# Performance work log

Measured on AMD Instinct MI355X. Metric: run time of the kernel, lower is better.

Reference implementation:

```python
import jax, jax.numpy as jnp
import numpy as np

DIM = 384
NUM_HEADS = 8
HEAD_DIM = DIM // NUM_HEADS
SCALE = HEAD_DIM ** -0.5
MLP_HIDDEN = int(DIM * 4.0)
EPS = 1e-6


def setup_inputs() -> dict:
    key = jax.random.key(0)
    ks = jax.random.split(key, 8)
    s = 0.02
    return {
        "x": jax.random.normal(ks[0], (2, DIM, 8, 16, 16), dtype=jnp.float32),
        "g1": jnp.ones((DIM,), jnp.float32),
        "b1": jnp.zeros((DIM,), jnp.float32),
        "Wqkv": jax.random.normal(ks[1], (DIM, 3 * DIM), jnp.float32) * s,  # no bias (qkv_bias=False)
        "Wo": jax.random.normal(ks[2], (DIM, DIM), jnp.float32) * s,
        "bo": jnp.zeros((DIM,), jnp.float32),
        "g2": jnp.ones((DIM,), jnp.float32),
        "b2": jnp.zeros((DIM,), jnp.float32),
        "W1": jax.random.normal(ks[3], (DIM, MLP_HIDDEN), jnp.float32) * s,
        "b1m": jnp.zeros((MLP_HIDDEN,), jnp.float32),
        "W2": jax.random.normal(ks[4], (MLP_HIDDEN, DIM), jnp.float32) * s,
        "b2m": jnp.zeros((DIM,), jnp.float32),
    }


def _layernorm(x, g, b):
    mu = jnp.mean(x, axis=-1, keepdims=True)
    var = jnp.mean(jnp.square(x - mu), axis=-1, keepdims=True)
    return (x - mu) * jax.lax.rsqrt(var + EPS) * g + b


def _attention(h, Wqkv, Wo, bo):
    B, N, C = h.shape
    qkv = h @ Wqkv  # [B, N, 3C]
    qkv = qkv.reshape(B, N, 3, NUM_HEADS, HEAD_DIM).transpose(2, 0, 3, 1, 4)
    q, k, v = qkv[0], qkv[1], qkv[2]  # each [B, H, N, d]
    att = jax.nn.softmax(jnp.einsum('bhxd,bhyd->bhxy', q, k) * SCALE, axis=-1)
    out = jnp.einsum('bhxy,bhyd->bhxd', att, v)  # [B, H, N, d]
    out = out.transpose(0, 2, 1, 3).reshape(B, N, C)
    return out @ Wo + bo


def reference(x, g1, b1, Wqkv, Wo, bo, g2, b2, W1, b1m, W2, b2m):
    B, C, D, H, W = x.shape
    h = x.transpose(0, 2, 3, 4, 1).reshape(B, D * H * W, C)  # b (d h w) c
    h = h + _attention(_layernorm(h, g1, b1), Wqkv, Wo, bo)
    m = _layernorm(h, g2, b2)
    m = jax.nn.gelu(m @ W1 + b1m, approximate=False) @ W2 + b2m
    h = h + m
    return h.reshape(B, D, H, W, C).transpose(0, 4, 1, 2, 3)
```

## Files before the change

### kernel.cpp

```cpp
#include <hip/hip_runtime.h>
#include <hip/hip_bf16.h>
#include <math.h>

#define DIM    384
#define NHEAD  8
#define HDIM   48
#define NTOK   2048
#define BATCH  2
#define TOKS   (BATCH * NTOK)
#define HIDDEN 1536

typedef __bf16 bf16x8 __attribute__((ext_vector_type(8)));
typedef float  f32x4  __attribute__((ext_vector_type(4)));
typedef unsigned short u16;

union bfu { __hip_bfloat16 h; u16 u; };

__device__ __forceinline__ void load_lds16(const void* g, void* l) {
    __builtin_amdgcn_global_load_lds(
        (const __attribute__((address_space(1))) void*)g,
        (__attribute__((address_space(3))) void*)l, 16, 0, 0);
}

__global__ __launch_bounds__(256) void wtrans_all(
    const float* __restrict__ Wqkv, const float* __restrict__ Wo,
    const float* __restrict__ W1,   const float* __restrict__ W2,
    __hip_bfloat16* __restrict__ WqkvT, __hip_bfloat16* __restrict__ WoT,
    __hip_bfloat16* __restrict__ W1T,   __hip_bfloat16* __restrict__ W2T) {
    __shared__ float t[32][33];
    int id = blockIdx.x;
    const float* src; __hip_bfloat16* dst; int R, C;
    if (id < 432)       { src = Wqkv; dst = WqkvT; R = 384;  C = 1152; }
    else if (id < 576)  { id -= 432;  src = Wo;    dst = WoT;  R = 384;  C = 384; }
    else if (id < 1152) { id -= 576;  src = W1;    dst = W1T;  R = 384;  C = 1536; }
    else                { id -= 1152; src = W2;    dst = W2T;  R = 1536; C = 384; }
    int tc = C / 32;
    int i0 = (id / tc) * 32, j0 = (id % tc) * 32;
    int tx = threadIdx.x & 31, ty = threadIdx.x >> 5;
#pragma unroll
    for (int k = 0; k < 32; k += 8)
        t[ty + k][tx] = src[(size_t)(i0 + ty + k) * C + j0 + tx];
    __syncthreads();
#pragma unroll
    for (int k = 0; k < 32; k += 8)
        dst[(size_t)(j0 + ty + k) * R + i0 + tx] = __float2bfloat16(t[tx][ty + k]);
}

__global__ __launch_bounds__(256) void tln(const float* __restrict__ x,
                                           const float* __restrict__ g,
                                           const float* __restrict__ bta,
                                           float* __restrict__ hOut,
                                           __hip_bfloat16* __restrict__ y) {
    __shared__ float t[384 * 33];
    int n0 = blockIdx.x * 32, b = blockIdx.y;
    const float* xb = x + (size_t)b * DIM * NTOK;
    int tid = threadIdx.x;
    for (int idx = tid; idx < 384 * 32; idx += 256) {
        int c = idx >> 5, n = idx & 31;
        t[c * 33 + n] = xb[(size_t)c * NTOK + n0 + n];
    }
    __syncthreads();
    int wid = tid >> 6, lane = tid & 63;
#pragma unroll
    for (int it = 0; it < 8; ++it) {
        int tl = it * 4 + wid;
        float v[6];
        float s = 0.f;
#pragma unroll
        for (int i = 0; i < 6; ++i) { v[i] = t[(lane + 64 * i) * 33 + tl]; s += v[i]; }
#pragma unroll
        for (int o = 32; o; o >>= 1) s += __shfl_xor(s, o, 64);
        float mu = s * (1.f / DIM);
        float s2 = 0.f;
#pragma unroll
        for (int i = 0; i < 6; ++i) { float d = v[i] - mu; s2 += d * d; }
#pragma unroll
        for (int o = 32; o; o >>= 1) s2 += __shfl_xor(s2, o, 64);
        float r = rsqrtf(s2 * (1.f / DIM) + 1e-6f);
        size_t tok = (size_t)b * NTOK + n0 + tl;
#pragma unroll
        for (int i = 0; i < 6; ++i) {
            int c = lane + 64 * i;
            hOut[tok * DIM + c] = v[i];
            y[tok * DIM + c] = __float2bfloat16((v[i] - mu) * r * g[c] + bta[c]);
        }
    }
}

__global__ __launch_bounds__(256) void vtile(const u16* __restrict__ qkv,
                                             unsigned int* __restrict__ vt32) {
    __shared__ u16 t[128 * 49];
    int k0 = blockIdx.x * 128;
    int bh = blockIdx.y;
    int b = bh >> 3, h = bh & 7;
    int tid = threadIdx.x;
    const u16* src = qkv + (size_t)(b * NTOK + k0) * 1152 + 768 + h * 48;
#pragma unroll
    for (int idx = tid; idx < 768; idx += 256) {
        int r = idx / 6, c = idx % 6;
        uint4 v = *(const uint4*)(src + (size_t)r * 1152 + c * 8);
        u16* dst = &t[r * 49 + c * 8];
        dst[0] = (u16)(v.x & 0xffff); dst[1] = (u16)(v.x >> 16);
        dst[2] = (u16)(v.y & 0xffff); dst[3] = (u16)(v.y >> 16);
        dst[4] = (u16)(v.z & 0xffff); dst[5] = (u16)(v.z >> 16);
        dst[6] = (u16)(v.w & 0xffff); dst[7] = (u16)(v.w >> 16);
    }
    __syncthreads();
    unsigned int* outb = vt32 + (((size_t)bh * 48) * 2048 + k0) / 2;
#pragma unroll
    for (int idx = tid; idx < 3072; idx += 256) {
        int d = idx >> 6, pp = idx & 63;
        int k1 = (pp >> 5) * 64 + (pp & 1) * 32 + ((pp >> 1) & 15);
        unsigned int lo = t[k1 * 49 + d];
        unsigned int hi = t[(k1 + 16) * 49 + d];
        outb[(size_t)d * 1024 + pp] = lo | (hi << 16);
    }
}

__global__ __launch_bounds__(256) void ln_kernel(const float* __restrict__ x,
                                                 const float* __restrict__ g,
                                                 const float* __restrict__ bta,
                                                 __hip_bfloat16* __restrict__ y) {
    int wid = threadIdx.x >> 6, lane = threadIdx.x & 63;
    int tok = blockIdx.x * 4 + wid;
    const float* xr = x + (size_t)tok * DIM;
    float v[6];
    float s = 0.f;
#pragma unroll
    for (int i = 0; i < 6; ++i) { v[i] = xr[lane + 64 * i]; s += v[i]; }
#pragma unroll
    for (int o = 32; o; o >>= 1) s += __shfl_xor(s, o, 64);
    float mu = s * (1.f / DIM);
    float s2 = 0.f;
#pragma unroll
    for (int i = 0; i < 6; ++i) { float d = v[i] - mu; s2 += d * d; }
#pragma unroll
    for (int o = 32; o; o >>= 1) s2 += __shfl_xor(s2, o, 64);
    float r = rsqrtf(s2 * (1.f / DIM) + 1e-6f);
    __hip_bfloat16* yr = y + (size_t)tok * DIM;
#pragma unroll
    for (int i = 0; i < 6; ++i) {
        int c = lane + 64 * i;
        yr[c] = __float2bfloat16((v[i] - mu) * r * g[c] + bta[c]);
    }
}

template<bool GELU, bool BF16OUT, bool TRANSOUT>
__global__ __launch_bounds__(256) void gemm_mfma(
    const __hip_bfloat16* __restrict__ A,
    const __hip_bfloat16* __restrict__ BT,
    const float* __restrict__ bias,
    const float* __restrict__ res,
    void* __restrict__ Cout,
    int M, int N, int K) {
    __shared__ __align__(16) u16 As[2][64 * 32];
    __shared__ __align__(16) u16 Bs[2][64 * 32];
    int bm = blockIdx.y * 64, bn = blockIdx.x * 64;
    int tid = threadIdx.x;
    int w = tid >> 6, l = tid & 63;
    int m0 = (w >> 1) * 32, n0 = (w & 1) * 32;
    int lm = l & 15, ksel = l >> 4;

    int row = tid >> 2, c16 = tid & 3;
    const __hip_bfloat16* ga = A  + (size_t)(bm + row) * K + c16 * 8;
    const __hip_bfloat16* gb = BT + (size_t)(bn + row) * K + c16 * 8;

    f32x4 acc[2][2] = {};
    for (int k0 = 0; k0 < K; k0 += 64) {
        load_lds16(ga + k0,      &As[0][tid * 8]);
        load_lds16(ga + k0 + 32, &As[1][tid * 8]);
        load_lds16(gb + k0,      &Bs[0][tid * 8]);
        load_lds16(gb + k0 + 32, &Bs[1][tid * 8]);
        __syncthreads();
#pragma unroll
        for (int kk = 0; kk < 2; ++kk) {
            bf16x8 af0 = *(const bf16x8*)&As[kk][(m0 +      lm) * 32 + ksel * 8];
            bf16x8 af1 = *(const bf16x8*)&As[kk][(m0 + 16 + lm) * 32 + ksel * 8];
            bf16x8 bf0 = *(const bf16x8*)&Bs[kk][(n0 +      lm) * 32 + ksel * 8];
            bf16x8 bf1 = *(const bf16x8*)&Bs[kk][(n0 + 16 + lm) * 32 + ksel * 8];
            acc[0][0] = __builtin_amdgcn_mfma_f32_16x16x32_bf16(af0, bf0, acc[0][0], 0, 0, 0);
            acc[0][1] = __builtin_amdgcn_mfma_f32_16x16x32_bf16(af0, bf1, acc[0][1], 0, 0, 0);
            acc[1][0] = __builtin_amdgcn_mfma_f32_16x16x32_bf16(af1, bf0, acc[1][0], 0, 0, 0);
            acc[1][1] = __builtin_amdgcn_mfma_f32_16x16x32_bf16(af1, bf1, acc[1][1], 0, 0, 0);
        }
        __syncthreads();
    }

    if constexpr (TRANSOUT) {
        __shared__ float ct[64 * 65];
#pragma unroll
        for (int i = 0; i < 2; ++i)
#pragma unroll
            for (int j = 0; j < 2; ++j)
#pragma unroll
                for (int r = 0; r < 4; ++r) {
                    int ml = m0 + i * 16 + ksel * 4 + r;
                    int cl = n0 + j * 16 + lm;
                    float v = acc[i][j][r];
                    if (bias) v += bias[bn + cl];
                    if (res)  v += res[(size_t)(bm + ml) * N + bn + cl];
                    ct[ml * 65 + cl] = v;
                }
        __syncthreads();
        int bb = bm >> 11, nb = bm & (NTOK - 1);
        float* outp = (float*)Cout + (size_t)bb * DIM * NTOK + nb;
#pragma unroll
        for (int cl = w; cl < 64; cl += 4)
            outp[(size_t)(bn + cl) * NTOK + l] = ct[l * 65 + cl];
    } else {
#pragma unroll
        for (int i = 0; i < 2; ++i)
#pragma unroll
            for (int j = 0; j < 2; ++j)
#pragma unroll
                for (int r = 0; r < 4; ++r) {
                    int rg = bm + m0 + i * 16 + ksel * 4 + r;
                    int cg = bn + n0 + j * 16 + lm;
                    float v = acc[i][j][r];
                    if (bias) v += bias[cg];
                    if (GELU) v = 0.5f * v * (1.f + erff(v * 0.7071067811865475f));
                    if (res)  v += res[(size_t)rg * N + cg];
                    if (BF16OUT)
                        ((__hip_bfloat16*)Cout)[(size_t)rg * N + cg] = __float2bfloat16(v);
                    else
                        ((float*)Cout)[(size_t)rg * N + cg] = v;
                }
    }
}

#define ATK 128
#define PSTR 136
__global__ __launch_bounds__(512) void attn_mfma(
    const u16* __restrict__ qkv,
    const u16* __restrict__ vt,
    __hip_bfloat16* __restrict__ outp) {
    __shared__ __align__(16) u16 Qs[64 * 72];
    __shared__ __align__(16) u16 Ks[128 * 72];
    __shared__ __align__(16) u16 Vs[48 * PSTR];
    __shared__ __align__(16) u16 Ps[64 * PSTR];
    const int q0 = blockIdx.x * 64;
    const int h = blockIdx.y, b = blockIdx.z;
    const int tid = threadIdx.x;
    const int w = tid >> 6, l = tid & 63, lm = l & 15, quad = l >> 4;
    const int qc = w >> 1, kh = w & 1;

    for (int idx = tid; idx < 128; idx += 512) {
        int r = idx >> 1, c = idx & 1;
        *(uint4*)&Qs[r * 72 + 48 + c * 8] = uint4{0, 0, 0, 0};
    }
    for (int idx = tid; idx < 256; idx += 512) {
        int r = idx >> 1, c = idx & 1;
        *(uint4*)&Ks[r * 72 + 48 + c * 8] = uint4{0, 0, 0, 0};
    }
    const u16* qbase = qkv + (size_t)(b * NTOK + q0) * 1152 + h * 48;
    for (int idx = tid; idx < 384; idx += 512) {
        int r = idx / 6, c = idx % 6;
        *(uint4*)&Qs[r * 72 + c * 8] = *(const uint4*)(qbase + (size_t)r * 1152 + c * 8);
    }
    __syncthreads();

    bf16x8 aq0 = *(const bf16x8*)&Qs[(qc * 16 + lm) * 72 +  0 + quad * 8];
    bf16x8 aq1 = *(const bf16x8*)&Qs[(qc * 16 + lm) * 72 + 32 + quad * 8];

    float l_i[4] = {0.f, 0.f, 0.f, 0.f};
    f32x4 o_acc[3] = {};

    const u16* kbase = qkv + (size_t)(b * NTOK) * 1152 + 384 + h * 48;
    const u16* vbase = vt + (size_t)(b * NHEAD + h) * 48 * 2048;
    const float sc2 = 0.14433756729740643f * 1.4426950408889634f;

    for (int kt = 0; kt < NTOK / ATK; ++kt) {
        __syncthreads();
#pragma unroll
        for (int idx = tid; idx < 768; idx += 512) {
            int r = idx / 6, c = idx % 6;
            *(uint4*)&Ks[r * 72 + c * 8] =
                *(const uint4*)(kbase + (size_t)(kt * ATK + r) * 1152 + c * 8);
        }
#pragma unroll
        for (int idx = tid; idx < 768; idx += 512) {
            int d = idx >> 4, c = idx & 15;
            *(uint4*)&Vs[d * PSTR + c * 8] =
                *(const uint4*)(vbase + (size_t)d * 2048 + kt * ATK + c * 8);
        }
        __syncthreads();

        f32x4 s[4];
#pragma unroll
        for (int ntp = 0; ntp < 4; ++ntp) {
            int nt = kh * 4 + ntp;
            bf16x8 kf0 = *(const bf16x8*)&Ks[(nt * 16 + lm) * 72 +  0 + quad * 8];
            bf16x8 kf1 = *(const bf16x8*)&Ks[(nt * 16 + lm) * 72 + 32 + quad * 8];
            f32x4 t = {};
            t = __builtin_amdgcn_mfma_f32_16x16x32_bf16(aq0, kf0, t, 0, 0, 0);
            t = __builtin_amdgcn_mfma_f32_16x16x32_bf16(aq1, kf1, t, 0, 0, 0);
            s[ntp] = t;
        }

#pragma unroll
        for (int r = 0; r < 4; ++r) {
            u16 pr[4];
#pragma unroll
            for (int ntp = 0; ntp < 4; ++ntp) {
                float p = exp2f(s[ntp][r] * sc2);
                l_i[r] += p;
                bfu cv; cv.h = __float2bfloat16(p);
                pr[ntp] = cv.u;
            }
            *(uint2*)&Ps[(qc * 16 + quad * 4 + r) * PSTR + kh * 64 + lm * 4] =
                *(const uint2*)pr;
        }

#pragma unroll
        for (int ksp = 0; ksp < 2; ++ksp) {
            int ks = kh * 2 + ksp;
            bf16x8 pf = *(const bf16x8*)&Ps[(qc * 16 + lm) * PSTR + ks * 32 + quad * 8];
#pragma unroll
            for (int nt = 0; nt < 3; ++nt) {
                bf16x8 vf = *(const bf16x8*)&Vs[(nt * 16 + lm) * PSTR + ks * 32 + quad * 8];
                o_acc[nt] = __builtin_amdgcn_mfma_f32_16x16x32_bf16(pf, vf, o_acc[nt], 0, 0, 0);
            }
        }
    }

    __syncthreads();
    float* red = (float*)Ks;
    if (kh == 1) {
        f32x4* base = (f32x4*)&red[(qc * 64 + l) * 16];
        base[0] = o_acc[0]; base[1] = o_acc[1]; base[2] = o_acc[2];
        f32x4 lv; lv[0] = l_i[0]; lv[1] = l_i[1]; lv[2] = l_i[2]; lv[3] = l_i[3];
        base[3] = lv;
    }
    __syncthreads();
    if (kh == 0) {
        f32x4* base = (f32x4*)&red[(qc * 64 + l) * 16];
        o_acc[0] += base[0]; o_acc[1] += base[1]; o_acc[2] += base[2];
        f32x4 lv = base[3];
#pragma unroll
        for (int r = 0; r < 4; ++r) {
            float lsum = l_i[r] + lv[r];
#pragma unroll
            for (int o = 8; o; o >>= 1) lsum += __shfl_xor(lsum, o, 64);
            float inv = 1.f / lsum;
#pragma unroll
            for (int nt = 0; nt < 3; ++nt)
                outp[(size_t)(b * NTOK + q0 + qc * 16 + quad * 4 + r) * DIM
                     + h * 48 + nt * 16 + lm]
                    = __float2bfloat16(o_acc[nt][r] * inv);
        }
    }
}

extern "C" void kernel_launch(void* const* d_in, const int* in_sizes, int n_in,
                              void* d_out, int out_size, void* d_ws, size_t ws_size,
                              hipStream_t stream) {
    const float* x    = (const float*)d_in[0];
    const float* g1   = (const float*)d_in[1];
    const float* b1   = (const float*)d_in[2];
    const float* Wqkv = (const float*)d_in[3];
    const float* Wo   = (const float*)d_in[4];
    const float* bo   = (const float*)d_in[5];
    const float* g2   = (const float*)d_in[6];
    const float* b2   = (const float*)d_in[7];
    const float* W1   = (const float*)d_in[8];
    const float* b1m  = (const float*)d_in[9];
    const float* W2   = (const float*)d_in[10];
    const float* b2m  = (const float*)d_in[11];
    float* out = (float*)d_out;

    char* p = (char*)d_ws;
    float* bufH = (float*)p;                       p += (size_t)TOKS * DIM * 4;
    char* qkvp = p;
    __hip_bfloat16* bufQKVb = (__hip_bfloat16*)p;  p += (size_t)TOKS * 3 * DIM * 2;
    __hip_bfloat16* bufVT   = (__hip_bfloat16*)p;  p += (size_t)TOKS * DIM * 2;
    __hip_bfloat16* bufNb   = (__hip_bfloat16*)p;  p += (size_t)TOKS * DIM * 2;
    __hip_bfloat16* bufAb   = (__hip_bfloat16*)p;  p += (size_t)TOKS * DIM * 2;
    __hip_bfloat16* WqkvT   = (__hip_bfloat16*)p;  p += (size_t)3 * DIM * DIM * 2;
    __hip_bfloat16* WoT     = (__hip_bfloat16*)p;  p += (size_t)DIM * DIM * 2;
    __hip_bfloat16* W1T     = (__hip_bfloat16*)p;  p += (size_t)HIDDEN * DIM * 2;
    __hip_bfloat16* W2T     = (__hip_bfloat16*)p;  p += (size_t)DIM * HIDDEN * 2;
    __hip_bfloat16* bufHIDb = (__hip_bfloat16*)qkvp;

    wtrans_all<<<1728, 256, 0, stream>>>(Wqkv, Wo, W1, W2, WqkvT, WoT, W1T, W2T);
    tln<<<dim3(NTOK / 32, BATCH), 256, 0, stream>>>(x, g1, b1, bufH, bufNb);
    gemm_mfma<false, true, false><<<dim3(3 * DIM / 64, TOKS / 64), 256, 0, stream>>>(
        bufNb, WqkvT, nullptr, nullptr, bufQKVb, TOKS, 3 * DIM, DIM);
    vtile<<<dim3(NTOK / 128, BATCH * NHEAD), 256, 0, stream>>>(
        (const u16*)bufQKVb, (unsigned int*)bufVT);
    attn_mfma<<<dim3(NTOK / 64, NHEAD, BATCH), 512, 0, stream>>>(
        (const u16*)bufQKVb, (const u16*)bufVT, bufAb);
    gemm_mfma<false, false, false><<<dim3(DIM / 64, TOKS / 64), 256, 0, stream>>>(
        bufAb, WoT, bo, bufH, bufH, TOKS, DIM, DIM);
    ln_kernel<<<TOKS / 4, 256, 0, stream>>>(bufH, g2, b2, bufNb);
    gemm_mfma<true, true, false><<<dim3(HIDDEN / 64, TOKS / 64), 256, 0, stream>>>(
        bufNb, W1T, b1m, nullptr, bufHIDb, TOKS, HIDDEN, DIM);
    gemm_mfma<false, false, true><<<dim3(DIM / 64, TOKS / 64), 256, 0, stream>>>(
        bufHIDb, W2T, b2m, bufH, out, TOKS, DIM, HIDDEN);
}
```

Baseline: 197.8 us.

## Merge weight-transpose with input layernorm, fuse V transpose into QKV GEMM epilogue

The weight transpose/convert and the transposed layernorm of x now run in one combined launch with a block-index split. The separate V-retiling kernel is removed: the QKV GEMM epilogue writes the V columns straight into the tiled transposed layout that attention expects. Attention also merges the Q and P shared buffers and adds an occupancy hint to launch_bounds. This saves two launches and one round trip of V through global memory, at the cost of scattered 2-byte stores in the GEMM epilogue and possible register pressure from the occupancy hint.

```diff
diff --git a/kernel.cpp b/kernel.cpp
--- a/kernel.cpp
+++ b/kernel.cpp
@@ -22,98 +22,69 @@
         (__attribute__((address_space(3))) void*)l, 16, 0, 0);
 }
 
-__global__ __launch_bounds__(256) void wtrans_all(
+__global__ __launch_bounds__(256) void prep(
     const float* __restrict__ Wqkv, const float* __restrict__ Wo,
     const float* __restrict__ W1,   const float* __restrict__ W2,
     __hip_bfloat16* __restrict__ WqkvT, __hip_bfloat16* __restrict__ WoT,
-    __hip_bfloat16* __restrict__ W1T,   __hip_bfloat16* __restrict__ W2T) {
-    __shared__ float t[32][33];
+    __hip_bfloat16* __restrict__ W1T,   __hip_bfloat16* __restrict__ W2T,
+    const float* __restrict__ x, const float* __restrict__ g,
+    const float* __restrict__ bta,
+    float* __restrict__ hOut, __hip_bfloat16* __restrict__ y) {
+    __shared__ __align__(16) char smem[384 * 33 * 4];
     int id = blockIdx.x;
-    const float* src; __hip_bfloat16* dst; int R, C;
-    if (id < 432)       { src = Wqkv; dst = WqkvT; R = 384;  C = 1152; }
-    else if (id < 576)  { id -= 432;  src = Wo;    dst = WoT;  R = 384;  C = 384; }
-    else if (id < 1152) { id -= 576;  src = W1;    dst = W1T;  R = 384;  C = 1536; }
-    else                { id -= 1152; src = W2;    dst = W2T;  R = 1536; C = 384; }
-    int tc = C / 32;
-    int i0 = (id / tc) * 32, j0 = (id % tc) * 32;
-    int tx = threadIdx.x & 31, ty = threadIdx.x >> 5;
-#pragma unroll
-    for (int k = 0; k < 32; k += 8)
-        t[ty + k][tx] = src[(size_t)(i0 + ty + k) * C + j0 + tx];
-    __syncthreads();
-#pragma unroll
-    for (int k = 0; k < 32; k += 8)
-        dst[(size_t)(j0 + ty + k) * R + i0 + tx] = __float2bfloat16(t[tx][ty + k]);
-}
-
-__global__ __launch_bounds__(256) void tln(const float* __restrict__ x,
-                                           const float* __restrict__ g,
-                                           const float* __restrict__ bta,
-                                           float* __restrict__ hOut,
-                                           __hip_bfloat16* __restrict__ y) {
-    __shared__ float t[384 * 33];
-    int n0 = blockIdx.x * 32, b = blockIdx.y;
-    const float* xb = x + (size_t)b * DIM * NTOK;
     int tid = threadIdx.x;
-    for (int idx = tid; idx < 384 * 32; idx += 256) {
-        int c = idx >> 5, n = idx & 31;
-        t[c * 33 + n] = xb[(size_t)c * NTOK + n0 + n];
-    }
-    __syncthreads();
-    int wid = tid >> 6, lane = tid & 63;
-#pragma unroll
-    for (int it = 0; it < 8; ++it) {
-        int tl = it * 4 + wid;
-        float v[6];
-        float s = 0.f;
-#pragma unroll
-        for (int i = 0; i < 6; ++i) { v[i] = t[(lane + 64 * i) * 33 + tl]; s += v[i]; }
-#pragma unroll
-        for (int o = 32; o; o >>= 1) s += __shfl_xor(s, o, 64);
-        float mu = s * (1.f / DIM);
-        float s2 = 0.f;
-#pragma unroll
-        for (int i = 0; i < 6; ++i) { float d = v[i] - mu; s2 += d * d; }
-#pragma unroll
-        for (int o = 32; o; o >>= 1) s2 += __shfl_xor(s2, o, 64);
-        float r = rsqrtf(s2 * (1.f / DIM) + 1e-6f);
-        size_t tok = (size_t)b * NTOK + n0 + tl;
-#pragma unroll
-        for (int i = 0; i < 6; ++i) {
-            int c = lane + 64 * i;
-            hOut[tok * DIM + c] = v[i];
-            y[tok * DIM + c] = __float2bfloat16((v[i] - mu) * r * g[c] + bta[c]);
-        }
-    }
-}
-
-__global__ __launch_bounds__(256) void vtile(const u16* __restrict__ qkv,
-                                             unsigned int* __restrict__ vt32) {
-    __shared__ u16 t[128 * 49];
-    int k0 = blockIdx.x * 128;
-    int bh = blockIdx.y;
-    int b = bh >> 3, h = bh & 7;
-    int tid = threadIdx.x;
-    const u16* src = qkv + (size_t)(b * NTOK + k0) * 1152 + 768 + h * 48;
-#pragma unroll
-    for (int idx = tid; idx < 768; idx += 256) {
-        int r = idx / 6, c = idx % 6;
-        uint4 v = *(const uint4*)(src + (size_t)r * 1152 + c * 8);
-        u16* dst = &t[r * 49 + c * 8];
-        dst[0] = (u16)(v.x & 0xffff); dst[1] = (u16)(v.x >> 16);
-        dst[2] = (u16)(v.y & 0xffff); dst[3] = (u16)(v.y >> 16);
-        dst[4] = (u16)(v.z & 0xffff); dst[5] = (u16)(v.z >> 16);
-        dst[6] = (u16)(v.w & 0xffff); dst[7] = (u16)(v.w >> 16);
-    }
-    __syncthreads();
-    unsigned int* outb = vt32 + (((size_t)bh * 48) * 2048 + k0) / 2;
-#pragma unroll
-    for (int idx = tid; idx < 3072; idx += 256) {
-        int d = idx >> 6, pp = idx & 63;
-        int k1 = (pp >> 5) * 64 + (pp & 1) * 32 + ((pp >> 1) & 15);
-        unsigned int lo = t[k1 * 49 + d];
-        unsigned int hi = t[(k1 + 16) * 49 + d];
-        outb[(size_t)d * 1024 + pp] = lo | (hi << 16);
+    if (id < 1728) {
+        float (*t)[33] = (float(*)[33])smem;
+        const float* src; __hip_bfloat16* dst; int R, C;
+        if (id < 432)       { src = Wqkv; dst = WqkvT; R = 384;  C = 1152; }
+        else if (id < 576)  { id -= 432;  src = Wo;    dst = WoT;  R = 384;  C = 384; }
+        else if (id < 1152) { id -= 576;  src = W1;    dst = W1T;  R = 384;  C = 1536; }
+        else                { id -= 1152; src = W2;    dst = W2T;  R = 1536; C = 384; }
+        int tc = C / 32;
+        int i0 = (id / tc) * 32, j0 = (id % tc) * 32;
+        int tx = tid & 31, ty = tid >> 5;
+#pragma unroll
+        for (int k = 0; k < 32; k += 8)
+            t[ty + k][tx] = src[(size_t)(i0 + ty + k) * C + j0 + tx];
+        __syncthreads();
+#pragma unroll
+        for (int k = 0; k < 32; k += 8)
+            dst[(size_t)(j0 + ty + k) * R + i0 + tx] = __float2bfloat16(t[tx][ty + k]);
+    } else {
+        float* t = (float*)smem;
+        int id2 = id - 1728;
+        int n0 = (id2 & 63) * 32, b = id2 >> 6;
+        const float* xb = x + (size_t)b * DIM * NTOK;
+        for (int idx = tid; idx < 384 * 32; idx += 256) {
+            int c = idx >> 5, n = idx & 31;
+            t[c * 33 + n] = xb[(size_t)c * NTOK + n0 + n];
+        }
+        __syncthreads();
+        int wid = tid >> 6, lane = tid & 63;
+#pragma unroll
+        for (int it = 0; it < 8; ++it) {
+            int tl = it * 4 + wid;
+            float v[6];
+            float s = 0.f;
+#pragma unroll
+            for (int i = 0; i < 6; ++i) { v[i] = t[(lane + 64 * i) * 33 + tl]; s += v[i]; }
+#pragma unroll
+            for (int o = 32; o; o >>= 1) s += __shfl_xor(s, o, 64);
+            float mu = s * (1.f / DIM);
+            float s2 = 0.f;
+#pragma unroll
+            for (int i = 0; i < 6; ++i) { float d = v[i] - mu; s2 += d * d; }
+#pragma unroll
+            for (int o = 32; o; o >>= 1) s2 += __shfl_xor(s2, o, 64);
+            float r = rsqrtf(s2 * (1.f / DIM) + 1e-6f);
+            size_t tok = (size_t)b * NTOK + n0 + tl;
+#pragma unroll
+            for (int i = 0; i < 6; ++i) {
+                int c = lane + 64 * i;
+                hOut[tok * DIM + c] = v[i];
+                y[tok * DIM + c] = __float2bfloat16((v[i] - mu) * r * g[c] + bta[c]);
+            }
+        }
     }
 }
 
@@ -145,14 +116,15 @@
     }
 }
 
-template<bool GELU, bool BF16OUT, bool TRANSOUT>
+template<bool GELU, bool BF16OUT, bool TRANSOUT, bool QKV>
 __global__ __launch_bounds__(256) void gemm_mfma(
     const __hip_bfloat16* __restrict__ A,
     const __hip_bfloat16* __restrict__ BT,
     const float* __restrict__ bias,
     const float* __restrict__ res,
     void* __restrict__ Cout,
-    int M, int N, int K) {
+    int M, int N, int K,
+    __hip_bfloat16* __restrict__ vtout) {
     __shared__ __align__(16) u16 As[2][64 * 32];
     __shared__ __align__(16) u16 Bs[2][64 * 32];
     int bm = blockIdx.y * 64, bn = blockIdx.x * 64;
@@ -220,24 +192,35 @@
                     if (bias) v += bias[cg];
                     if (GELU) v = 0.5f * v * (1.f + erff(v * 0.7071067811865475f));
                     if (res)  v += res[(size_t)rg * N + cg];
-                    if (BF16OUT)
+                    if constexpr (QKV) {
+                        if (cg < 768) {
+                            ((__hip_bfloat16*)Cout)[(size_t)rg * 1152 + cg] = __float2bfloat16(v);
+                        } else {
+                            int c = cg - 768, hh = c / 48, dd = c - hh * 48;
+                            int bb = rg >> 11, n = rg & (NTOK - 1);
+                            int kk = n & 127;
+                            int pos = ((kk >> 6) << 6) + ((kk & 15) << 2) + ((kk >> 4) & 3);
+                            vtout[((size_t)(bb * NHEAD + hh) * 48 + dd) * 2048
+                                  + (n & ~127) + pos] = __float2bfloat16(v);
+                        }
+                    } else if constexpr (BF16OUT) {
                         ((__hip_bfloat16*)Cout)[(size_t)rg * N + cg] = __float2bfloat16(v);
-                    else
+                    } else {
                         ((float*)Cout)[(size_t)rg * N + cg] = v;
+                    }
                 }
     }
 }
 
 #define ATK 128
 #define PSTR 136
-__global__ __launch_bounds__(512) void attn_mfma(
+__global__ __launch_bounds__(512, 6) void attn_mfma(
     const u16* __restrict__ qkv,
     const u16* __restrict__ vt,
     __hip_bfloat16* __restrict__ outp) {
-    __shared__ __align__(16) u16 Qs[64 * 72];
+    __shared__ __align__(16) u16 PQ[64 * PSTR];
     __shared__ __align__(16) u16 Ks[128 * 72];
     __shared__ __align__(16) u16 Vs[48 * PSTR];
-    __shared__ __align__(16) u16 Ps[64 * PSTR];
     const int q0 = blockIdx.x * 64;
     const int h = blockIdx.y, b = blockIdx.z;
     const int tid = threadIdx.x;
@@ -246,7 +229,7 @@
 
     for (int idx = tid; idx < 128; idx += 512) {
         int r = idx >> 1, c = idx & 1;
-        *(uint4*)&Qs[r * 72 + 48 + c * 8] = uint4{0, 0, 0, 0};
+        *(uint4*)&PQ[r * 72 + 48 + c * 8] = uint4{0, 0, 0, 0};
     }
     for (int idx = tid; idx < 256; idx += 512) {
         int r = idx >> 1, c = idx & 1;
@@ -255,12 +238,12 @@
     const u16* qbase = qkv + (size_t)(b * NTOK + q0) * 1152 + h * 48;
     for (int idx = tid; idx < 384; idx += 512) {
         int r = idx / 6, c = idx % 6;
-        *(uint4*)&Qs[r * 72 + c * 8] = *(const uint4*)(qbase + (size_t)r * 1152 + c * 8);
+        *(uint4*)&PQ[r * 72 + c * 8] = *(const uint4*)(qbase + (size_t)r * 1152 + c * 8);
     }
     __syncthreads();
 
-    bf16x8 aq0 = *(const bf16x8*)&Qs[(qc * 16 + lm) * 72 +  0 + quad * 8];
-    bf16x8 aq1 = *(const bf16x8*)&Qs[(qc * 16 + lm) * 72 + 32 + quad * 8];
+    bf16x8 aq0 = *(const bf16x8*)&PQ[(qc * 16 + lm) * 72 +  0 + quad * 8];
+    bf16x8 aq1 = *(const bf16x8*)&PQ[(qc * 16 + lm) * 72 + 32 + quad * 8];
 
     float l_i[4] = {0.f, 0.f, 0.f, 0.f};
     f32x4 o_acc[3] = {};
@@ -307,14 +290,14 @@
                 bfu cv; cv.h = __float2bfloat16(p);
                 pr[ntp] = cv.u;
             }
-            *(uint2*)&Ps[(qc * 16 + quad * 4 + r) * PSTR + kh * 64 + lm * 4] =
+            *(uint2*)&PQ[(qc * 16 + quad * 4 + r) * PSTR + kh * 64 + lm * 4] =
                 *(const uint2*)pr;
         }
 
 #pragma unroll
         for (int ksp = 0; ksp < 2; ++ksp) {
             int ks = kh * 2 + ksp;
-            bf16x8 pf = *(const bf16x8*)&Ps[(qc * 16 + lm) * PSTR + ks * 32 + quad * 8];
+            bf16x8 pf = *(const bf16x8*)&PQ[(qc * 16 + lm) * PSTR + ks * 32 + quad * 8];
 #pragma unroll
             for (int nt = 0; nt < 3; ++nt) {
                 bf16x8 vf = *(const bf16x8*)&Vs[(nt * 16 + lm) * PSTR + ks * 32 + quad * 8];
@@ -381,19 +364,17 @@
     __hip_bfloat16* W2T     = (__hip_bfloat16*)p;  p += (size_t)DIM * HIDDEN * 2;
     __hip_bfloat16* bufHIDb = (__hip_bfloat16*)qkvp;
 
-    wtrans_all<<<1728, 256, 0, stream>>>(Wqkv, Wo, W1, W2, WqkvT, WoT, W1T, W2T);
-    tln<<<dim3(NTOK / 32, BATCH), 256, 0, stream>>>(x, g1, b1, bufH, bufNb);
-    gemm_mfma<false, true, false><<<dim3(3 * DIM / 64, TOKS / 64), 256, 0, stream>>>(
-        bufNb, WqkvT, nullptr, nullptr, bufQKVb, TOKS, 3 * DIM, DIM);
-    vtile<<<dim3(NTOK / 128, BATCH * NHEAD), 256, 0, stream>>>(
-        (const u16*)bufQKVb, (unsigned int*)bufVT);
+    prep<<<1728 + 128, 256, 0, stream>>>(Wqkv, Wo, W1, W2, WqkvT, WoT, W1T, W2T,
+                                         x, g1, b1, bufH, bufNb);
+    gemm_mfma<false, true, false, true><<<dim3(3 * DIM / 64, TOKS / 64), 256, 0, stream>>>(
+        bufNb, WqkvT, nullptr, nullptr, bufQKVb, TOKS, 3 * DIM, DIM, bufVT);
     attn_mfma<<<dim3(NTOK / 64, NHEAD, BATCH), 512, 0, stream>>>(
         (const u16*)bufQKVb, (const u16*)bufVT, bufAb);
-    gemm_mfma<false, false, false><<<dim3(DIM / 64, TOKS / 64), 256, 0, stream>>>(
-        bufAb, WoT, bo, bufH, bufH, TOKS, DIM, DIM);
+    gemm_mfma<false, false, false, false><<<dim3(DIM / 64, TOKS / 64), 256, 0, stream>>>(
+        bufAb, WoT, bo, bufH, bufH, TOKS, DIM, DIM, nullptr);
     ln_kernel<<<TOKS / 4, 256, 0, stream>>>(bufH, g2, b2, bufNb);
-    gemm_mfma<true, true, false><<<dim3(HIDDEN / 64, TOKS / 64), 256, 0, stream>>>(
-        bufNb, W1T, b1m, nullptr, bufHIDb, TOKS, HIDDEN, DIM);
-    gemm_mfma<false, false, true><<<dim3(DIM / 64, TOKS / 64), 256, 0, stream>>>(
-        bufHIDb, W2T, b2m, bufH, out, TOKS, DIM, HIDDEN);
-}
+    gemm_mfma<true, true, false, false><<<dim3(HIDDEN / 64, TOKS / 64), 256, 0, stream>>>(
+        bufNb, W1T, b1m, nullptr, bufHIDb, TOKS, HIDDEN, DIM, nullptr);
+    gemm_mfma<false, false, true, false><<<dim3(DIM / 64, TOKS / 64), 256, 0, stream>>>(
+        bufHIDb, W2T, b2m, bufH, out, TOKS, DIM, HIDDEN, nullptr);
+}
```

Result: no change. 198.1 us, median of 3 (+0.1%).
